# Kernel optimization log

Measured on AMD Instinct MI355X. Metric: run time of the kernel, lower is better.

## Reference

```python
import jax, jax.numpy as jnp
import numpy as np

B, S, D = 2, 2048, 1024
H, KS, VS = 16, 64, 64

def setup_inputs() -> dict:
    key = jax.random.key(0)
    ks = jax.random.split(key, 11)
    s = 1.0 / np.sqrt(D)
    return {
        "query": jax.random.normal(ks[0], (B, S, D), jnp.float32),
        "key":   jax.random.normal(ks[1], (B, S, D), jnp.float32),
        "value": jax.random.normal(ks[2], (B, S, D), jnp.float32),
        # weights stored [in, out] (transpose of torch Linear)
        "Wq": jax.random.normal(ks[3], (D, H * KS), jnp.float32) * s,
        "bq": jnp.zeros((H * KS,), jnp.float32),
        "Wk": jax.random.normal(ks[4], (D, H * KS), jnp.float32) * s,
        "bk": jnp.zeros((H * KS,), jnp.float32),
        "Wv": jax.random.normal(ks[5], (D, H * VS), jnp.float32) * s,
        "bv": jnp.zeros((H * VS,), jnp.float32),
        "Wo": jax.random.normal(ks[6], (H * VS, D), jnp.float32) * s,
        "bo": jnp.zeros((D,), jnp.float32),
    }

def reference(query, key, value, Wq, bq, Wk, bk, Wv, bv, Wo, bo):
    b = query.shape[0]
    # projections + split heads -> [B, H, S, d]
    Q = (query @ Wq + bq).reshape(b, -1, H, KS).transpose(0, 2, 1, 3)
    K = (key   @ Wk + bk).reshape(b, -1, H, KS).transpose(0, 2, 1, 3)
    V = (value @ Wv + bv).reshape(b, -1, H, VS).transpose(0, 2, 1, 3)
    scores = jnp.einsum('bhqd,bhkd->bhqk', Q, K) / jnp.sqrt(jnp.float32(KS))
    attn = jax.nn.softmax(scores, axis=-1)  # dropout_rate=0.0 -> identity
    ctx = jnp.einsum('bhqk,bhkd->bhqd', attn, V)  # [B,H,S,VS]
    ctx = ctx.transpose(0, 2, 1, 3).reshape(b, attn.shape[-1], H * VS)
    out = ctx @ Wo + bo
    return out, attn
```

## Files before the change

kernel.cpp:

```cpp
#include <hip/hip_runtime.h>
#include <stdint.h>


typedef _Float16 f16;
typedef f16 f16x4 __attribute__((ext_vector_type(4)));
typedef f16 f16x8 __attribute__((ext_vector_type(8)));
typedef float f32x4 __attribute__((ext_vector_type(4)));
typedef uint32_t u32;
typedef u32 u32x4 __attribute__((ext_vector_type(4)));

#define L2E 1.4426950408889634f

__device__ __forceinline__ void gload16(const void* g, void* l) {
    __builtin_amdgcn_global_load_lds((__attribute__((address_space(1))) void*)g,
                                     (__attribute__((address_space(3))) void*)l,
                                     16, 0, 0);
}

__global__ __launch_bounds__(256) void k_cvt(const float* __restrict__ q,
                                             const float* __restrict__ k,
                                             const float* __restrict__ v,
                                             f16* __restrict__ dst)
{
    int z = blockIdx.z;
    const float* s = (z == 0) ? q : (z == 1) ? k : v;
    size_t i = (size_t)blockIdx.x * 256 + threadIdx.x;
    float4 f = ((const float4*)s)[i];
    f16x4 o = {(f16)f.x, (f16)f.y, (f16)f.z, (f16)f.w};
    *(f16x4*)(dst + (size_t)z * 4194304 + i * 4) = o;
}

__global__ __launch_bounds__(256) void k_wtrans(const float* __restrict__ w0,
                                                const float* __restrict__ w1,
                                                const float* __restrict__ w2,
                                                const float* __restrict__ w3,
                                                f16* __restrict__ wt)
{
    __shared__ f16 t[64][72];
    int z = blockIdx.z;
    const float* W = (z == 0) ? w0 : (z == 1) ? w1 : (z == 2) ? w2 : w3;
    f16* outp = wt + (size_t)z * 1048576;
    int tx = blockIdx.x, ty = blockIdx.y, tid = threadIdx.x;
#pragma unroll
    for (int r4 = 0; r4 < 4; r4++) {
        int row = r4 * 16 + (tid >> 4);
        int col = (tid & 15) * 4;
        float4 f = *(const float4*)(W + (size_t)(ty * 64 + row) * 1024 + tx * 64 + col);
        t[col + 0][row] = (f16)f.x; t[col + 1][row] = (f16)f.y;
        t[col + 2][row] = (f16)f.z; t[col + 3][row] = (f16)f.w;
    }
    __syncthreads();
#pragma unroll
    for (int cc = 0; cc < 2; cc++) {
        int c = tid + cc * 256;
        int row = c >> 3, ch = c & 7;
        f16x8 vv;
#pragma unroll
        for (int j = 0; j < 8; j++) vv[j] = t[row][ch * 8 + j];
        *(f16x8*)(outp + (size_t)(tx * 64 + row) * 1024 + ty * 64 + ch * 8) = vv;
    }
}

__global__ __launch_bounds__(256) void k_gemm(const f16* __restrict__ Ab,
                                              const f16* __restrict__ Wtb,
                                              const float* __restrict__ b0,
                                              const float* __restrict__ b1,
                                              const float* __restrict__ b2,
                                              void* __restrict__ o0,
                                              void* __restrict__ o1,
                                              int proj)
{
    __shared__ __align__(16) char As[16384];
    __shared__ __align__(16) char Bs[16384];
    const int tid = threadIdx.x;
    const int wv = tid >> 6, ln = tid & 63, lg = ln >> 4, li = ln & 15;
    const int m0 = blockIdx.y * 128, n0 = blockIdx.x * 128;
    const int wm = (wv >> 1) * 64, wn = (wv & 1) * 64;

    const f16* A; const f16* Bt; const float* bias; int mode;
    if (proj) {
        int z = blockIdx.z;
        A = Ab + (size_t)z * 4194304;
        Bt = Wtb + (size_t)z * 1048576;
        bias = (z == 0) ? b0 : (z == 1) ? b1 : b2;
        mode = (z == 2) ? 1 : 0;
    } else { A = Ab; Bt = Wtb; bias = b0; mode = 2; }

    const char* gA[4]; const char* gB[4];
#pragma unroll
    for (int c = 0; c < 4; c++) {
        int r = (wv * 4 + c) * 8 + (ln >> 3);
        int j = (ln & 7) ^ (r & 7);
        gA[c] = (const char*)A  + (size_t)(m0 + r) * 2048 + j * 16;
        gB[c] = (const char*)Bt + (size_t)(n0 + r) * 2048 + j * 16;
    }

    f32x4 acc[4][4] = {};
    for (int kt = 0; kt < 16; kt++) {
        __syncthreads();
#pragma unroll
        for (int c = 0; c < 4; c++) {
            gload16(gA[c] + kt * 128, As + (wv * 4 + c) * 1024);
            gload16(gB[c] + kt * 128, Bs + (wv * 4 + c) * 1024);
        }
        __syncthreads();
#pragma unroll
        for (int kk = 0; kk < 2; kk++) {
            f16x8 af[4], bf[4];
#pragma unroll
            for (int mi = 0; mi < 4; mi++) {
                int row = wm + mi * 16 + li;
                af[mi] = *(const f16x8*)(As + row * 128 + (((kk * 4 + lg) ^ (row & 7)) * 16));
            }
#pragma unroll
            for (int ni = 0; ni < 4; ni++) {
                int row = wn + ni * 16 + li;
                bf[ni] = *(const f16x8*)(Bs + row * 128 + (((kk * 4 + lg) ^ (row & 7)) * 16));
            }
#pragma unroll
            for (int mi = 0; mi < 4; mi++)
#pragma unroll
                for (int ni = 0; ni < 4; ni++)
                    acc[mi][ni] = __builtin_amdgcn_mfma_f32_16x16x32_f16(af[mi], bf[ni], acc[mi][ni], 0, 0, 0);
        }
    }

    float bvs[4];
#pragma unroll
    for (int ni = 0; ni < 4; ni++) bvs[ni] = bias[n0 + wn + ni * 16 + li];

    if (mode == 2) {
        float* O = (float*)o0;
#pragma unroll
        for (int mi = 0; mi < 4; mi++)
#pragma unroll
            for (int ni = 0; ni < 4; ni++) {
                int n = n0 + wn + ni * 16 + li;
#pragma unroll
                for (int r = 0; r < 4; r++) {
                    int m = m0 + wm + mi * 16 + lg * 4 + r;
                    O[(size_t)m * 1024 + n] = acc[mi][ni][r] + bvs[ni];
                }
            }
    } else if (mode == 0) {
        f16* O = (f16*)o0 + (size_t)blockIdx.z * 4194304;
#pragma unroll
        for (int mi = 0; mi < 4; mi++)
#pragma unroll
            for (int ni = 0; ni < 4; ni++) {
                int n = n0 + wn + ni * 16 + li;
                int h = n >> 6, d = n & 63;
#pragma unroll
                for (int r = 0; r < 4; r++) {
                    int m = m0 + wm + mi * 16 + lg * 4 + r;
                    int b = m >> 11, s = m & 2047;
                    O[(((size_t)b * 16 + h) * 2048 + s) * 64 + d] = (f16)(acc[mi][ni][r] + bvs[ni]);
                }
            }
    } else {
        f16* O = (f16*)o1;
#pragma unroll
        for (int mi = 0; mi < 4; mi++)
#pragma unroll
            for (int ni = 0; ni < 4; ni++) {
                int n = n0 + wn + ni * 16 + li;
                int h = n >> 6, d = n & 63;
                int mb = m0 + wm + mi * 16 + lg * 4;
                int b = mb >> 11, s = mb & 2047;
                f16x4 pk;
#pragma unroll
                for (int r = 0; r < 4; r++) pk[r] = (f16)(acc[mi][ni][r] + bvs[ni]);
                *(f16x4*)(O + (((size_t)b * 16 + h) * 64 + d) * 2048 + s) = pk;
            }
    }
}

__global__ __launch_bounds__(256, 4) void k_attn(const f16* __restrict__ Qb,
                                                 const f16* __restrict__ Kb,
                                                 const f16* __restrict__ Vt,
                                                 float* __restrict__ attn,
                                                 f16* __restrict__ ctx)
{
    __shared__ __align__(16) char Ks[16384];
    __shared__ __align__(16) char Ps[4][2048];
    const int tid = threadIdx.x, wv = tid >> 6, ln = tid & 63, lg = ln >> 4, li = ln & 15;
    const int bid = blockIdx.x;
    const int kk = bid >> 3;
    const int bh = (bid & 7) * 4 + (kk >> 5);
    const int q0 = (kk & 31) * 64 + wv * 16;

    const char* KbB = (const char*)Kb + (size_t)bh * 262144;
    const char* VtB = (const char*)Vt + (size_t)bh * 262144;

    const f16* qrow = Qb + ((size_t)bh * 2048 + q0 + li) * 64 + lg * 8;
    f16x8 aq0 = *(const f16x8*)(qrow);
    f16x8 aq1 = *(const f16x8*)(qrow + 32);
#pragma unroll
    for (int j = 0; j < 8; j++) {
        aq0[j] = (f16)((float)aq0[j] * 0.125f);
        aq1[j] = (f16)((float)aq1[j] * 0.125f);
    }

    float lacc[4] = {0.f, 0.f, 0.f, 0.f};
    {
        int swp[4];
        const char* gp[4];
#pragma unroll
        for (int t = 0; t < 4; t++) {
            int c = tid + t * 256;
            int r = c >> 3, j = c & 7;
            swp[t] = r * 128 + ((j ^ (r & 7)) * 16);
            gp[t] = KbB + (size_t)r * 128 + j * 16;
        }
        u32x4 s[4];
#pragma unroll
        for (int t = 0; t < 4; t++) s[t] = *(const u32x4*)(gp[t]);
        for (int kt = 0; kt < 16; kt++) {
            __syncthreads();
#pragma unroll
            for (int t = 0; t < 4; t++) *(u32x4*)(Ks + swp[t]) = s[t];
            __syncthreads();
            if (kt + 1 < 16) {
#pragma unroll
                for (int t = 0; t < 4; t++) s[t] = *(const u32x4*)(gp[t] + (size_t)(kt + 1) * 16384);
            }
#pragma unroll
            for (int cf = 0; cf < 8; cf++) {
                int row = cf * 16 + li;
                f16x8 ak0 = *(const f16x8*)(Ks + row * 128 + ((lg ^ (row & 7)) * 16));
                f16x8 ak1 = *(const f16x8*)(Ks + row * 128 + (((4 + lg) ^ (row & 7)) * 16));
                f32x4 z = {0.f, 0.f, 0.f, 0.f};
                z = __builtin_amdgcn_mfma_f32_16x16x32_f16(ak0, aq0, z, 0, 0, 0);
                z = __builtin_amdgcn_mfma_f32_16x16x32_f16(ak1, aq1, z, 0, 0, 0);
                lacc[cf & 3] += exp2f(z[0] * L2E) + exp2f(z[1] * L2E)
                              + exp2f(z[2] * L2E) + exp2f(z[3] * L2E);
            }
        }
    }
    float l_ = (lacc[0] + lacc[1]) + (lacc[2] + lacc[3]);
    l_ += __shfl_xor(l_, 16);
    l_ += __shfl_xor(l_, 32);
    const float inv_l = 1.0f / l_;
    float* aBase = attn + ((size_t)bh * 2048 + q0) * 2048;
    char* Pw = Ps[wv];

    const int srowb = ln >> 4;
    const int skv = (ln & 15) * 4;
    const int sldso = (((ln & 15) >> 1) * 16) + (ln & 1) * 8;

    f32x4 cacc[4] = {};
    const int r0 = tid >> 3, j0 = tid & 7;
    const int r1 = (tid + 256) >> 3, j1 = (tid + 256) & 7;
    const int sw0 = r0 * 128 + ((j0 ^ (r0 & 7)) * 16);
    const int sw1 = r1 * 128 + ((j1 ^ (r1 & 7)) * 16);
    u32x4 sk0 = *(const u32x4*)(KbB + (size_t)r0 * 128 + j0 * 16);
    u32x4 sk1 = *(const u32x4*)(KbB + (size_t)r1 * 128 + j1 * 16);
    for (int kt = 0; kt < 32; kt++) {
        __syncthreads();
        *(u32x4*)(Ks + sw0) = sk0;
        *(u32x4*)(Ks + sw1) = sk1;
        __syncthreads();
        if (kt + 1 < 32) {
            sk0 = *(const u32x4*)(KbB + (size_t)((kt + 1) * 64 + r0) * 128 + j0 * 16);
            sk1 = *(const u32x4*)(KbB + (size_t)((kt + 1) * 64 + r1) * 128 + j1 * 16);
        }
        f16x8 vf[4][2];
#pragma unroll
        for (int df = 0; df < 4; df++) {
            const char* vr = VtB + (size_t)(df * 16 + li) * 4096 + kt * 128 + lg * 16;
            vf[df][0] = *(const f16x8*)vr;
            vf[df][1] = *(const f16x8*)(vr + 64);
        }
        f32x4 zz[4];
#pragma unroll
        for (int cf = 0; cf < 4; cf++) {
            int row = cf * 16 + li;
            f16x8 ak0 = *(const f16x8*)(Ks + row * 128 + ((lg ^ (row & 7)) * 16));
            f16x8 ak1 = *(const f16x8*)(Ks + row * 128 + (((4 + lg) ^ (row & 7)) * 16));
            f32x4 z = {0.f, 0.f, 0.f, 0.f};
            z = __builtin_amdgcn_mfma_f32_16x16x32_f16(ak0, aq0, z, 0, 0, 0);
            z = __builtin_amdgcn_mfma_f32_16x16x32_f16(ak1, aq1, z, 0, 0, 0);
            zz[cf] = z;
        }
#pragma unroll
        for (int cf = 0; cf < 4; cf++) {
            float p0 = exp2f(zz[cf][0] * L2E) * inv_l;
            float p1 = exp2f(zz[cf][1] * L2E) * inv_l;
            float p2 = exp2f(zz[cf][2] * L2E) * inv_l;
            float p3 = exp2f(zz[cf][3] * L2E) * inv_l;
            f16x4 pk = {(f16)p0, (f16)p1, (f16)p2, (f16)p3};
            int c = cf * 2 + (lg >> 1);
            *(f16x4*)(Pw + li * 128 + ((c ^ (li & 7)) * 16) + (lg & 1) * 8) = pk;
        }
#pragma unroll
        for (int j = 0; j < 4; j++) {
            int row = j * 4 + srowb;
            f16x4 pv4 = *(const f16x4*)(Pw + row * 128 + (sldso ^ ((row & 7) * 16)));
            f32x4 fv = {(float)pv4[0], (float)pv4[1], (float)pv4[2], (float)pv4[3]};
            __builtin_nontemporal_store(fv, (f32x4*)(aBase + (size_t)row * 2048 + kt * 64 + skv));
        }
#pragma unroll
        for (int s2 = 0; s2 < 2; s2++) {
            f16x8 bp = *(const f16x8*)(Pw + li * 128 + (((s2 * 4 + lg) ^ (li & 7)) * 16));
#pragma unroll
            for (int df = 0; df < 4; df++)
                cacc[df] = __builtin_amdgcn_mfma_f32_16x16x32_f16(vf[df][s2], bp, cacc[df], 0, 0, 0);
        }
    }

    const int b = bh >> 4, h = bh & 15;
#pragma unroll
    for (int df = 0; df < 4; df++) {
        f16x4 pk;
#pragma unroll
        for (int r = 0; r < 4; r++) pk[r] = (f16)cacc[df][r];
        size_t mrow = (size_t)b * 2048 + q0 + li;
        size_t n = (size_t)h * 64 + df * 16 + lg * 4;
        *(f16x4*)(ctx + mrow * 1024 + n) = pk;
    }
}

extern "C" void kernel_launch(void* const* d_in, const int* in_sizes, int n_in,
                              void* d_out, int out_size, void* d_ws, size_t ws_size,
                              hipStream_t stream)
{
    const float* q  = (const float*)d_in[0];
    const float* k  = (const float*)d_in[1];
    const float* v  = (const float*)d_in[2];
    const float* Wq = (const float*)d_in[3];
    const float* bq = (const float*)d_in[4];
    const float* Wk = (const float*)d_in[5];
    const float* bk = (const float*)d_in[6];
    const float* Wv = (const float*)d_in[7];
    const float* bv = (const float*)d_in[8];
    const float* Wo = (const float*)d_in[9];
    const float* bo = (const float*)d_in[10];

    f16* W = (f16*)d_ws;
    float* out = (float*)d_out;
    float* attn = out + 4194304;

    f16* X   = W;
    f16* Wt  = W + 12582912;
    f16* QKb = W + 16777216;
    f16* Vt  = W + 25165824;
    f16* ctx = W + 29360128;

    k_cvt<<<dim3(4096, 1, 3), 256, 0, stream>>>(q, k, v, X);
    k_wtrans<<<dim3(16, 16, 4), 256, 0, stream>>>(Wq, Wk, Wv, Wo, Wt);
    k_gemm<<<dim3(8, 32, 3), 256, 0, stream>>>(X, Wt, bq, bk, bv, QKb, Vt, 1);
    k_attn<<<dim3(1024), 256, 0, stream>>>(QKb, QKb + 4194304, Vt, attn, ctx);
    k_gemm<<<dim3(8, 32, 1), 256, 0, stream>>>(ctx, Wt + 3145728, bo, bo, bo, out, nullptr, 0);
}
```

Baseline: 257.8 us.

## Merge prep kernels, fold Q scale into Wq, remap GEMM tiles for XCD locality

```diff
diff --git a/kernel.cpp b/kernel.cpp
--- a/kernel.cpp
+++ b/kernel.cpp
@@ -17,37 +17,42 @@
                                      16, 0, 0);
 }
 
-__global__ __launch_bounds__(256) void k_cvt(const float* __restrict__ q,
-                                             const float* __restrict__ k,
-                                             const float* __restrict__ v,
-                                             f16* __restrict__ dst)
-{
-    int z = blockIdx.z;
-    const float* s = (z == 0) ? q : (z == 1) ? k : v;
-    size_t i = (size_t)blockIdx.x * 256 + threadIdx.x;
-    float4 f = ((const float4*)s)[i];
-    f16x4 o = {(f16)f.x, (f16)f.y, (f16)f.z, (f16)f.w};
-    *(f16x4*)(dst + (size_t)z * 4194304 + i * 4) = o;
-}
-
-__global__ __launch_bounds__(256) void k_wtrans(const float* __restrict__ w0,
-                                                const float* __restrict__ w1,
-                                                const float* __restrict__ w2,
-                                                const float* __restrict__ w3,
-                                                f16* __restrict__ wt)
+__global__ __launch_bounds__(256) void k_prep(const float* __restrict__ q,
+                                              const float* __restrict__ k,
+                                              const float* __restrict__ v,
+                                              const float* __restrict__ w0,
+                                              const float* __restrict__ w1,
+                                              const float* __restrict__ w2,
+                                              const float* __restrict__ w3,
+                                              f16* __restrict__ dst,
+                                              f16* __restrict__ wt)
 {
     __shared__ f16 t[64][72];
-    int z = blockIdx.z;
+    const int bid = blockIdx.x, tid = threadIdx.x;
+    if (bid < 12288) {
+        int z = bid >> 12;
+        int bx = bid & 4095;
+        const float* s = (z == 0) ? q : (z == 1) ? k : v;
+        size_t i = (size_t)bx * 256 + tid;
+        float4 f = ((const float4*)s)[i];
+        f16x4 o = {(f16)f.x, (f16)f.y, (f16)f.z, (f16)f.w};
+        *(f16x4*)(dst + (size_t)z * 4194304 + i * 4) = o;
+        return;
+    }
+    int w = bid - 12288;
+    int z = w >> 8;
+    int rem = w & 255;
+    int tx = rem & 15, ty = rem >> 4;
     const float* W = (z == 0) ? w0 : (z == 1) ? w1 : (z == 2) ? w2 : w3;
+    const float ws = (z == 0) ? 0.125f : 1.0f;
     f16* outp = wt + (size_t)z * 1048576;
-    int tx = blockIdx.x, ty = blockIdx.y, tid = threadIdx.x;
 #pragma unroll
     for (int r4 = 0; r4 < 4; r4++) {
         int row = r4 * 16 + (tid >> 4);
         int col = (tid & 15) * 4;
         float4 f = *(const float4*)(W + (size_t)(ty * 64 + row) * 1024 + tx * 64 + col);
-        t[col + 0][row] = (f16)f.x; t[col + 1][row] = (f16)f.y;
-        t[col + 2][row] = (f16)f.z; t[col + 3][row] = (f16)f.w;
+        t[col + 0][row] = (f16)(f.x * ws); t[col + 1][row] = (f16)(f.y * ws);
+        t[col + 2][row] = (f16)(f.z * ws); t[col + 3][row] = (f16)(f.w * ws);
     }
     __syncthreads();
 #pragma unroll
@@ -74,15 +79,19 @@
     __shared__ __align__(16) char Bs[16384];
     const int tid = threadIdx.x;
     const int wv = tid >> 6, ln = tid & 63, lg = ln >> 4, li = ln & 15;
-    const int m0 = blockIdx.y * 128, n0 = blockIdx.x * 128;
+    const int lin = blockIdx.x + (blockIdx.y << 3);
+    const int xcd = lin & 7, loc = lin >> 3;
+    const int m0 = (xcd * 4 + (loc >> 3)) * 128;
+    const int n0 = (loc & 7) * 128;
     const int wm = (wv >> 1) * 64, wn = (wv & 1) * 64;
 
-    const f16* A; const f16* Bt; const float* bias; int mode;
+    const f16* A; const f16* Bt; const float* bias; int mode; float bscale = 1.0f;
     if (proj) {
         int z = blockIdx.z;
         A = Ab + (size_t)z * 4194304;
         Bt = Wtb + (size_t)z * 1048576;
         bias = (z == 0) ? b0 : (z == 1) ? b1 : b2;
+        if (z == 0) bscale = 0.125f;
         mode = (z == 2) ? 1 : 0;
     } else { A = Ab; Bt = Wtb; bias = b0; mode = 2; }
 
@@ -127,7 +136,7 @@
 
     float bvs[4];
 #pragma unroll
-    for (int ni = 0; ni < 4; ni++) bvs[ni] = bias[n0 + wn + ni * 16 + li];
+    for (int ni = 0; ni < 4; ni++) bvs[ni] = bias[n0 + wn + ni * 16 + li] * bscale;
 
     if (mode == 2) {
         float* O = (float*)o0;
@@ -195,11 +204,6 @@
     const f16* qrow = Qb + ((size_t)bh * 2048 + q0 + li) * 64 + lg * 8;
     f16x8 aq0 = *(const f16x8*)(qrow);
     f16x8 aq1 = *(const f16x8*)(qrow + 32);
-#pragma unroll
-    for (int j = 0; j < 8; j++) {
-        aq0[j] = (f16)((float)aq0[j] * 0.125f);
-        aq1[j] = (f16)((float)aq1[j] * 0.125f);
-    }
 
     float lacc[4] = {0.f, 0.f, 0.f, 0.f};
     {
@@ -346,8 +350,7 @@
     f16* Vt  = W + 25165824;
     f16* ctx = W + 29360128;
 
-    k_cvt<<<dim3(4096, 1, 3), 256, 0, stream>>>(q, k, v, X);
-    k_wtrans<<<dim3(16, 16, 4), 256, 0, stream>>>(Wq, Wk, Wv, Wo, Wt);
+    k_prep<<<dim3(13312), 256, 0, stream>>>(q, k, v, Wq, Wk, Wv, Wo, X, Wt);
     k_gemm<<<dim3(8, 32, 3), 256, 0, stream>>>(X, Wt, bq, bk, bv, QKb, Vt, 1);
     k_attn<<<dim3(1024), 256, 0, stream>>>(QKb, QKb + 4194304, Vt, attn, ctx);
     k_gemm<<<dim3(8, 32, 1), 256, 0, stream>>>(ctx, Wt + 3145728, bo, bo, bo, out, nullptr, 0);
```

After: 253.3 us. About the same (-1.7%).
